# Kernel tuning notes

Measured on AMD Instinct MI355X. Metric: run time of the kernel, lower is better.

## Reference

```python
import jax, jax.numpy as jnp
import numpy as np

FACTORS = (16, 8, 8)          # prod == n_embd == 1024
H, DK = 16, 64
FACTOR_PARAMS = tuple(f * (f - 1) // 2 for f in FACTORS)  # (120, 28, 28)
DV = sum(FACTOR_PARAMS)       # 176
DVP = 256                     # next power of two padding
B, T, C = 2, 2048, 1024
OFFSET = 64


def _skew_exp(params, f):
    """params: (..., f*(f-1)//2) -> rotation matrices (..., f, f) via expm of skew-sym."""
    rows, cols = np.triu_indices(f, k=1)
    batch = params.shape[:-1]
    mat = jnp.zeros(batch + (f, f), jnp.float32).at[..., rows, cols].set(params.astype(jnp.float32))
    S = mat - jnp.swapaxes(mat, -1, -2)
    R = jax.vmap(jax.scipy.linalg.expm)(S.reshape((-1, f, f)))
    return R.reshape(batch + (f, f))


def setup_inputs() -> dict:
    key = jax.random.key(0)
    k1, k2, k3, k4, k5 = jax.random.split(key, 5)
    return {
        "x": jax.random.normal(k1, (B, T, C), jnp.float32),
        "cached_k": jax.random.normal(k2, (B, H, OFFSET, DK), jnp.float32),
        "cached_v": jax.random.normal(k3, (B, H, OFFSET, DVP), jnp.float32),
        "W_QK": jax.random.normal(k4, (2 * H * DK, C), jnp.float32) * 0.02,
        "W_V": jax.random.normal(k5, (H * DV, C), jnp.float32) * 0.02,
    }


def reference(x, cached_k, cached_v, W_QK, W_V):
    Bx, Tx, Cx = x.shape
    qk = x @ W_QK.T                                  # (B,T,2*H*DK)
    q, k = jnp.split(qk, 2, axis=-1)
    q = q.reshape(Bx, Tx, H, DK).transpose(0, 2, 1, 3)   # (B,H,T,DK)
    k = k.reshape(Bx, Tx, H, DK).transpose(0, 2, 1, 3)
    v = (x @ W_V.T).reshape(Bx, Tx, H, DV).transpose(0, 2, 1, 3)  # (B,H,T,DV)
    v = jnp.pad(v, ((0, 0), (0, 0), (0, 0), (0, DVP - DV)))       # pad to DVP

    offset = cached_k.shape[2]
    k = jnp.concatenate([cached_k, k], axis=2)       # (B,H,offset+T,DK)
    v = jnp.concatenate([cached_v, v], axis=2)       # (B,H,offset+T,DVP)

    neg_inf = jnp.finfo(jnp.float32).min
    causal = jnp.triu(jnp.full((Tx, Tx), neg_inf, jnp.float32), k=1)
    mask = jnp.concatenate([jnp.zeros((Tx, offset), jnp.float32), causal], axis=1)

    scores = jnp.einsum('bhqd,bhkd->bhqk', q, k) * (1.0 / np.sqrt(DK)) + mask
    attn = jax.nn.softmax(scores, axis=-1)
    rot = jnp.einsum('bhqk,bhkd->bhqd', attn, v)[..., :DV]   # (B,H,T,DV)
    rot = rot.transpose(0, 2, 1, 3).sum(axis=2)              # sum over heads -> (B,T,DV)

    splits = jnp.split(rot, np.cumsum(FACTOR_PARAMS)[:-1].tolist(), axis=-1)
    y = x.reshape(Bx, Tx, *FACTORS)
    for i, (p, f) in enumerate(zip(splits, FACTORS)):
        R = _skew_exp(p, f).astype(x.dtype)          # (B,T,f,f)
        y = jnp.moveaxis(y, 2 + i, 2)
        sh = y.shape
        y = (R @ y.reshape(Bx, Tx, f, -1)).reshape(sh)
        y = jnp.moveaxis(y, 2, 2 + i)
    y = y.reshape(Bx, Tx, Cx)
    return y, k, v
```

## Files before the change

### kernel.cpp

```cpp
#include <hip/hip_runtime.h>

typedef _Float16 h8 __attribute__((ext_vector_type(8)));
typedef _Float16 h4 __attribute__((ext_vector_type(4)));
typedef float f4 __attribute__((ext_vector_type(4)));

#define NB 2
#define NT 2048
#define NC 1024
#define NH 16
#define DKK 64
#define DV 176
#define DVP 256
#define OFF 64
#define KV 2112
#define SCALE_Q 0.18033688011112f
#define CLAMP_S 11.541560327111f

__device__ __forceinline__ void load_lds16(const _Float16* g, _Float16* l) {
    __builtin_amdgcn_global_load_lds(
        (const __attribute__((address_space(1))) void*)g,
        (__attribute__((address_space(3))) void*)l, 16, 0, 0);
}

#define PREPA_X   1048576
#define PREPA_QK  1572864
#define PREPA_WV  2293760
#define PREPA_END 2473984
__global__ __launch_bounds__(256)
void k_prep_a(const float* __restrict__ x, const float* __restrict__ wqk,
              const float* __restrict__ wv, _Float16* __restrict__ xh,
              _Float16* __restrict__ wqkh, _Float16* __restrict__ wvh,
              float* __restrict__ rotb) {
    int i = blockIdx.x * 256 + threadIdx.x;
    if (i >= PREPA_END) return;
    if (i < PREPA_X) {
        float4 v = *(const float4*)(x + (size_t)i * 4);
        h4 h = {(_Float16)v.x, (_Float16)v.y, (_Float16)v.z, (_Float16)v.w};
        *(h4*)(xh + (size_t)i * 4) = h;
    } else if (i < PREPA_QK) {
        int j = i - PREPA_X;
        float4 v = *(const float4*)(wqk + (size_t)j * 4);
        h4 h = {(_Float16)v.x, (_Float16)v.y, (_Float16)v.z, (_Float16)v.w};
        *(h4*)(wqkh + (size_t)j * 4) = h;
    } else if (i < PREPA_WV) {
        int j = i - PREPA_QK;
        float4 v = *(const float4*)(wv + (size_t)j * 4);
        h4 h = {(_Float16)v.x, (_Float16)v.y, (_Float16)v.z, (_Float16)v.w};
        *(h4*)(wvh + (size_t)j * 4) = h;
    } else {
        int j = i - PREPA_WV;
        *(float4*)(rotb + (size_t)j * 4) = (float4){0.f, 0.f, 0.f, 0.f};
    }
}

#define PREPB_CK   32768
#define PREPB_CV   163840
#define PREPB_END  1474560
__global__ __launch_bounds__(256)
void k_prep_b(const float* __restrict__ ck, const float* __restrict__ cv,
              float* __restrict__ out_k, _Float16* __restrict__ kh,
              float* __restrict__ out_v, _Float16* __restrict__ vTh) {
    int i = blockIdx.x * 256 + threadIdx.x;
    if (i >= PREPB_END) return;
    if (i < PREPB_CK) {
        int bh = i >> 10, rem = i & 1023;
        int pos = rem >> 4, d4 = (rem & 15) * 4;
        float4 v = *(const float4*)(ck + (size_t)i * 4);
        size_t o = ((size_t)bh * KV + pos) * DKK + d4;
        *(float4*)(out_k + o) = v;
        h4 h = {(_Float16)v.x, (_Float16)v.y, (_Float16)v.z, (_Float16)v.w};
        *(h4*)(kh + o) = h;
    } else if (i < PREPB_CV) {
        int j = i - PREPB_CK;
        int bh = j >> 12, rem = j & 4095;
        int pos = rem >> 6, c4 = (rem & 63) * 4;
        float4 v = *(const float4*)(cv + (size_t)j * 4);
        *(float4*)(out_v + ((size_t)bh * KV + pos) * DVP + c4) = v;
        if (c4 < DV) {
            _Float16* vt = vTh + ((size_t)bh * DV + c4) * KV + pos;
            vt[0]              = (_Float16)v.x;
            vt[KV]             = (_Float16)v.y;
            vt[2 * (size_t)KV] = (_Float16)v.z;
            vt[3 * (size_t)KV] = (_Float16)v.w;
        }
    } else {
        int j = i - PREPB_CV;
        int bh = j / 40960, rem = j - bh * 40960;
        int t = rem / 20, c4 = DV + (rem - t * 20) * 4;
        *(float4*)(out_v + ((size_t)bh * KV + OFF + t) * DVP + c4) = (float4){0.f, 0.f, 0.f, 0.f};
    }
}

__global__ __launch_bounds__(256)
void k_gemm_fused(const _Float16* __restrict__ xh, const _Float16* __restrict__ wh,
                  _Float16* __restrict__ qh, _Float16* __restrict__ kh,
                  float* __restrict__ out_k, _Float16* __restrict__ vTh,
                  float* __restrict__ out_v) {
    __shared__ char smem_raw[65536];
    auto Ts = (_Float16(*)[64][72])smem_raw;
    auto Tq = (_Float16(*)[128][68])smem_raw;

    const int tid = threadIdx.x;
    const int lane = tid & 63, w = tid >> 6;
    const int lr = lane & 15, lg = lane >> 4;
    const int wm = w >> 1, wn = w & 1;
    const int n = blockIdx.x, x = n & 7, idx = n >> 3;
    const int c_  = idx >> 6;
    const int loc = idx & 63;
    const int mi = (x & 3) * 8 + (loc & 7);
    const int ni = (x >> 2) * 19 + c_ * 8 + (loc >> 3);
    const int m0 = mi * 128, n0 = ni * 128;
    const int srow = lane >> 3;
    const int sc16 = (lane & 7) ^ srow;

    f4 acc[4][4];
#pragma unroll
    for (int i = 0; i < 4; i++)
#pragma unroll
        for (int j = 0; j < 4; j++) acc[i][j] = (f4){0.f, 0.f, 0.f, 0.f};

    auto stage = [&](int buf, int k0) {
        _Float16* Ab = (_Float16*)smem_raw + buf * 8192;
        _Float16* Bb = (_Float16*)(smem_raw + 32768) + buf * 8192;
#pragma unroll
        for (int j = 0; j < 4; j++) {
            int i = w * 4 + j;
            int row = i * 8 + srow;
            load_lds16(&xh[(size_t)(m0 + row) * NC + k0 + sc16 * 8], Ab + i * 512);
            load_lds16(&wh[(size_t)(n0 + row) * NC + k0 + sc16 * 8], Bb + i * 512);
        }
    };

    stage(0, 0);
    int cur = 0;
    for (int t = 0; t < 16; ++t) {
        if (t < 15) {
            stage(cur ^ 1, (t + 1) * 64);
            asm volatile("s_waitcnt vmcnt(8)" ::: "memory");
        } else {
            asm volatile("s_waitcnt vmcnt(0)" ::: "memory");
        }
        __builtin_amdgcn_s_barrier();
        __builtin_amdgcn_sched_barrier(0);

        const _Float16* Ab = (const _Float16*)smem_raw + cur * 8192;
        const _Float16* Bb = (const _Float16*)(smem_raw + 32768) + cur * 8192;
#pragma unroll
        for (int ks = 0; ks < 2; ks++) {
            h8 a[4], b[4];
#pragma unroll
            for (int mt = 0; mt < 4; mt++) {
                int row = wm * 64 + mt * 16 + lr;
                a[mt] = *(const h8*)&Ab[row * 64 + ((ks * 4 + lg) ^ (lr & 7)) * 8];
            }
#pragma unroll
            for (int nt = 0; nt < 4; nt++) {
                int row = wn * 64 + nt * 16 + lr;
                b[nt] = *(const h8*)&Bb[row * 64 + ((ks * 4 + lg) ^ (lr & 7)) * 8];
            }
            __builtin_amdgcn_s_setprio(1);
#pragma unroll
            for (int mt = 0; mt < 4; mt++)
#pragma unroll
                for (int nt = 0; nt < 4; nt++)
                    acc[mt][nt] = __builtin_amdgcn_mfma_f32_16x16x32_f16(a[mt], b[nt], acc[mt][nt], 0, 0, 0);
            __builtin_amdgcn_s_setprio(0);
        }
        __builtin_amdgcn_sched_barrier(0);
        __builtin_amdgcn_s_barrier();
        cur ^= 1;
    }

    const int b_ = m0 >> 11;
    const int mloc = m0 & (NT - 1);

    if (ni < 8) {
        __syncthreads();
#pragma unroll
        for (int mt = 0; mt < 4; mt++)
#pragma unroll
            for (int nt = 0; nt < 4; nt++)
#pragma unroll
                for (int r = 0; r < 4; r++)
                    Tq[wn][wm * 64 + mt * 16 + lg * 4 + r][nt * 16 + lr] =
                        (_Float16)(acc[mt][nt][r] * SCALE_Q);
        __syncthreads();
        const int h0 = n0 >> 6;
#pragma unroll
        for (int i = 0; i < 8; i++) {
            int id = i * 256 + tid;
            int hh = id >> 10, rem = id & 1023;
            int t = rem >> 3, dk8 = (rem & 7) * 8;
            h8 v = *(const h8*)&Tq[hh][t][dk8];
            *(h8*)&qh[((size_t)(b_ * NH + h0 + hh) * NT + mloc + t) * DKK + dk8] = v;
        }
    } else if (ni < 16) {
        __syncthreads();
#pragma unroll
        for (int mt = 0; mt < 4; mt++)
#pragma unroll
            for (int nt = 0; nt < 4; nt++)
#pragma unroll
                for (int r = 0; r < 4; r++) {
                    int t = wm * 64 + mt * 16 + lg * 4 + r;
                    int g2 = n0 - 1024 + wn * 64 + nt * 16 + lr;
                    float v = acc[mt][nt][r];
                    int h = g2 >> 6, dk = g2 & 63;
                    out_k[((size_t)(b_ * NH + h) * KV + OFF + mloc + t) * DKK + dk] = v;
                    Tq[wn][t][nt * 16 + lr] = (_Float16)v;
                }
        __syncthreads();
        const int h0 = (n0 - 1024) >> 6;
#pragma unroll
        for (int i = 0; i < 8; i++) {
            int id = i * 256 + tid;
            int hh = id >> 10, rem = id & 1023;
            int t = rem >> 3, dk8 = (rem & 7) * 8;
            h8 v = *(const h8*)&Tq[hh][t][dk8];
            *(h8*)&kh[((size_t)(b_ * NH + h0 + hh) * KV + OFF + mloc + t) * DKK + dk8] = v;
        }
    } else {
        __syncthreads();
#pragma unroll
        for (int mt = 0; mt < 4; mt++)
#pragma unroll
            for (int nt = 0; nt < 4; nt++) {
                h4 ph;
#pragma unroll
                for (int r = 0; r < 4; r++) {
                    int grow = m0 + wm * 64 + mt * 16 + lg * 4 + r;
                    int gcol = n0 - 2048 + wn * 64 + nt * 16 + lr;
                    float v = acc[mt][nt][r];
                    int bb = grow >> 11, t = grow & (NT - 1);
                    int h = gcol / DV;
                    int c = gcol - h * DV;
                    out_v[((size_t)(bb * NH + h) * KV + OFF + t) * DVP + c] = v;
                    ph[r] = (_Float16)v;
                }
                *(h4*)&Ts[w][nt * 16 + lr][mt * 16 + lg * 4] = ph;
            }
        __syncthreads();
        {
            _Float16* vout = vTh + ((size_t)b_ * (NH * DV) + (n0 - 2048)) * KV + OFF + mloc;
            const int seg = tid & 31;
            const int rr = tid >> 5;
#pragma unroll
            for (int i = 0; i < 16; i++) {
                int c = i * 8 + rr;
                int buf = ((seg >> 4) << 1) | (c >> 6);
                h4 vv = *(const h4*)&Ts[buf][c & 63][(seg & 15) * 4];
                *(h4*)&vout[(size_t)c * KV + seg * 4] = vv;
            }
        }
    }
}

__global__ __launch_bounds__(256, 2)
void k_attn(const _Float16* __restrict__ qh, const _Float16* __restrict__ kh,
            const _Float16* __restrict__ vTh, float* __restrict__ rot) {
    __shared__ _Float16 Ks[2][64][64];
    __shared__ _Float16 Vs[2][176][64];
    __shared__ _Float16 Ps[4][16][72];
    const int tid = threadIdx.x, lane = tid & 63, w = tid >> 6;
    const int lr = lane & 15, lg = lane >> 4;
    const int n = blockIdx.x;
    const int gq = 31 - (n >> 5);
    const int bh = (n & 7) + 8 * ((n >> 3) & 3);
    const int b_ = bh >> 4;
    const int qt = gq * 4 + w;
    const int q = qt * 16 + lr;

    const _Float16* qp = qh + ((size_t)bh * NT + q) * DKK;
    h8 bq0 = *(const h8*)(qp + lg * 8);
    h8 bq1 = *(const h8*)(qp + 32 + lg * 8);

    const _Float16* kbase = kh + (size_t)bh * KV * DKK;
    const _Float16* vbase = vTh + (size_t)bh * DV * KV;

    f4 o[11];
#pragma unroll
    for (int i = 0; i < 11; i++) o[i] = (f4){0.f, 0.f, 0.f, 0.f};
    float l_acc = 0.f;

    const int nkt = gq + 2;
    const int srow = lane >> 3, sslot = lane & 7;
    const int sc16 = sslot ^ srow;

    auto stage = [&](int buf, int kt) {
#pragma unroll
        for (int t = 0; t < 8; t++) {
            int i = w * 8 + t;
            if (i > 29) i = 29;
            if (i < 8) {
                int row = i * 8 + srow;
                load_lds16(&kbase[(size_t)(kt * 64 + row) * DKK + sc16 * 8],
                           (_Float16*)Ks[buf] + i * 512);
            } else {
                int j = i - 8;
                int row = j * 8 + srow;
                load_lds16(&vbase[(size_t)row * KV + kt * 64 + sc16 * 8],
                           (_Float16*)Vs[buf] + j * 512);
            }
        }
    };

    stage(0, 0);
    int cur = 0;

    for (int kt = 0; kt < nkt; kt++) {
        if (kt + 1 < nkt) {
            stage(cur ^ 1, kt + 1);
            asm volatile("s_waitcnt vmcnt(8)" ::: "memory");
        } else {
            asm volatile("s_waitcnt vmcnt(0)" ::: "memory");
        }
        __builtin_amdgcn_s_barrier();
        __builtin_amdgcn_sched_barrier(0);

        f4 s[4];
        __builtin_amdgcn_s_setprio(1);
#pragma unroll
        for (int nt = 0; nt < 4; nt++) {
            int krow = nt * 16 + lr;
            h8 ak0 = *(const h8*)&Ks[cur][krow][(lg ^ (lr & 7)) * 8];
            h8 ak1 = *(const h8*)&Ks[cur][krow][((4 + lg) ^ (lr & 7)) * 8];
            f4 st = (f4){0.f, 0.f, 0.f, 0.f};
            st = __builtin_amdgcn_mfma_f32_16x16x32_f16(ak0, bq0, st, 0, 0, 0);
            st = __builtin_amdgcn_mfma_f32_16x16x32_f16(ak1, bq1, st, 0, 0, 0);
            s[nt] = st;
        }
        __builtin_amdgcn_s_setprio(0);

        if (kt + 1 < nkt) {
#pragma unroll
            for (int nt = 0; nt < 4; nt++) {
                h4 ph;
#pragma unroll
                for (int r = 0; r < 4; r++) {
                    float p = __builtin_exp2f(fminf(s[nt][r], CLAMP_S));
                    l_acc += p;
                    ph[r] = (_Float16)p;
                }
                *(h4*)&Ps[w][lr][nt * 16 + lg * 4] = ph;
            }
        } else {
#pragma unroll
            for (int nt = 0; nt < 4; nt++) {
                h4 ph;
#pragma unroll
                for (int r = 0; r < 4; r++) {
                    int key = kt * 64 + nt * 16 + lg * 4 + r;
                    float sv = fminf(s[nt][r], CLAMP_S);
                    float p = (key <= q + OFF) ? __builtin_exp2f(sv) : 0.f;
                    l_acc += p;
                    ph[r] = (_Float16)p;
                }
                *(h4*)&Ps[w][lr][nt * 16 + lg * 4] = ph;
            }
        }

        __builtin_amdgcn_s_setprio(1);
#pragma unroll
        for (int ks = 0; ks < 2; ks++) {
            h8 ap = *(const h8*)&Ps[w][lr][ks * 32 + lg * 8];
#pragma unroll
            for (int nt = 0; nt < 11; nt++) {
                int vrow = nt * 16 + lr;
                h8 bv = *(const h8*)&Vs[cur][vrow][((ks * 4 + lg) ^ (lr & 7)) * 8];
                o[nt] = __builtin_amdgcn_mfma_f32_16x16x32_f16(ap, bv, o[nt], 0, 0, 0);
            }
        }
        __builtin_amdgcn_s_setprio(0);
        __builtin_amdgcn_sched_barrier(0);
        __builtin_amdgcn_s_barrier();
        cur ^= 1;
    }

    l_acc += __shfl_xor(l_acc, 16);
    l_acc += __shfl_xor(l_acc, 32);
    float lq[4];
#pragma unroll
    for (int r = 0; r < 4; r++) lq[r] = 1.f / __shfl(l_acc, lg * 4 + r);
#pragma unroll
    for (int r = 0; r < 4; r++) {
        int t = qt * 16 + lg * 4 + r;
#pragma unroll
        for (int nt = 0; nt < 11; nt++) {
            atomicAdd(&rot[((size_t)b_ * NT + t) * DV + nt * 16 + lr], o[nt][r] * lq[r]);
        }
    }
}

__device__ __forceinline__ int triu16(int r, int c) { return r * 15 - (r * (r - 1)) / 2 + (c - r - 1); }
__device__ __forceinline__ int triu8(int r, int c)  { return r * 7  - (r * (r - 1)) / 2 + (c - r - 1); }

__global__ __launch_bounds__(64)
void k_rotate(const float* __restrict__ x, const float* __restrict__ rot,
              float* __restrict__ y) {
    __shared__ float A16[16][16], Ta[16][16], Tb[16][16];
    __shared__ float A8[2][8][8], T8a[2][8][8], T8b[2][8][8];
    __shared__ float pbuf[176];
    __shared__ float xt[1024], t1[1024], t2[1024];
    const int tok = blockIdx.x;
    const int lane = threadIdx.x;

    for (int i = lane; i < 176; i += 64) pbuf[i] = rot[(size_t)tok * DV + i];
    for (int i = lane; i < 1024; i += 64) xt[i] = x[(size_t)tok * NC + i];
    __syncthreads();

#pragma unroll
    for (int j = 0; j < 4; j++) {
        int e = lane * 4 + j, r = e >> 4, c = e & 15;
        float v = 0.f;
        if (r < c) v = pbuf[triu16(r, c)];
        else if (r > c) v = -pbuf[triu16(c, r)];
        A16[r][c] = v;
    }
    const int r8 = lane >> 3, c8 = lane & 7;
    {
#pragma unroll
        for (int m = 0; m < 2; m++) {
            float v = 0.f;
            if (r8 < c8) v = pbuf[120 + m * 28 + triu8(r8, c8)];
            else if (r8 > c8) v = -pbuf[120 + m * 28 + triu8(c8, r8)];
            A8[m][r8][c8] = v;
        }
    }
    __syncthreads();

    float rn = 0.f;
    if (lane < 16) {
#pragma unroll
        for (int c = 0; c < 16; c++) rn += fabsf(A16[lane][c]);
    }
#pragma unroll
    for (int mm = 1; mm < 16; mm <<= 1) rn = fmaxf(rn, __shfl_xor(rn, mm));
    rn = __shfl(rn, 0);
    int s16 = 0;
    while (rn > 0.5f && s16 < 60) { rn *= 0.5f; s16++; }

    int s8v[2];
#pragma unroll
    for (int m = 0; m < 2; m++) {
        float rn8 = 0.f;
        if (lane < 8) {
#pragma unroll
            for (int cc = 0; cc < 8; cc++) rn8 += fabsf(A8[m][lane][cc]);
        }
#pragma unroll
        for (int mm = 1; mm < 8; mm <<= 1) rn8 = fmaxf(rn8, __shfl_xor(rn8, mm));
        rn8 = __shfl(rn8, 0);
        int s8 = 0;
        while (rn8 > 0.5f && s8 < 60) { rn8 *= 0.5f; s8++; }
        s8v[m] = s8;
    }
    const float sc16 = exp2f((float)(-s16));
    const float sc80 = exp2f((float)(-s8v[0]));
    const float sc81 = exp2f((float)(-s8v[1]));
    __syncthreads();

#pragma unroll
    for (int j = 0; j < 4; j++) {
        int e = lane * 4 + j, r = e >> 4, c = e & 15;
        A16[r][c] *= sc16;
    }
    A8[0][r8][c8] *= sc80;
    A8[1][r8][c8] *= sc81;
    __syncthreads();
#pragma unroll
    for (int j = 0; j < 4; j++) {
        int e = lane * 4 + j, r = e >> 4, c = e & 15;
        Ta[r][c] = (r == c ? 1.f : 0.f) + A16[r][c] * (1.f / 12.f);
    }
    T8a[0][r8][c8] = (r8 == c8 ? 1.f : 0.f) + A8[0][r8][c8] * (1.f / 12.f);
    T8a[1][r8][c8] = (r8 == c8 ? 1.f : 0.f) + A8[1][r8][c8] * (1.f / 12.f);
    __syncthreads();

    float (*Tc)[16] = Ta, (*Tn)[16] = Tb;
    float (*tc0)[8] = T8a[0], (*tn0)[8] = T8b[0];
    float (*tc1)[8] = T8a[1], (*tn1)[8] = T8b[1];

    for (int k = 11; k >= 1; k--) {
        float inv_k = 1.f / (float)k;
#pragma unroll
        for (int j = 0; j < 4; j++) {
            int e = lane * 4 + j, r = e >> 4, c = e & 15;
            float acc = 0.f;
#pragma unroll
            for (int qv = 0; qv < 16; qv++) acc += A16[r][qv] * Tc[qv][c];
            Tn[r][c] = acc * inv_k + (r == c ? 1.f : 0.f);
        }
        {
            float a0 = 0.f, a1 = 0.f;
#pragma unroll
            for (int qv = 0; qv < 8; qv++) {
                a0 += A8[0][r8][qv] * tc0[qv][c8];
                a1 += A8[1][r8][qv] * tc1[qv][c8];
            }
            tn0[r8][c8] = a0 * inv_k + (r8 == c8 ? 1.f : 0.f);
            tn1[r8][c8] = a1 * inv_k + (r8 == c8 ? 1.f : 0.f);
        }
        __syncthreads();
        { float (*t)[16] = Tc; Tc = Tn; Tn = t; }
        { float (*t)[8] = tc0; tc0 = tn0; tn0 = t; }
        { float (*t)[8] = tc1; tc1 = tn1; tn1 = t; }
    }

    int smax = s16 > s8v[0] ? s16 : s8v[0];
    if (s8v[1] > smax) smax = s8v[1];
    for (int it = 0; it < smax; it++) {
        if (it < s16) {
#pragma unroll
            for (int j = 0; j < 4; j++) {
                int e = lane * 4 + j, r = e >> 4, c = e & 15;
                float acc = 0.f;
#pragma unroll
                for (int qv = 0; qv < 16; qv++) acc += Tc[r][qv] * Tc[qv][c];
                Tn[r][c] = acc;
            }
        }
        if (it < s8v[0]) {
            float a0 = 0.f;
#pragma unroll
            for (int qv = 0; qv < 8; qv++) a0 += tc0[r8][qv] * tc0[qv][c8];
            tn0[r8][c8] = a0;
        }
        if (it < s8v[1]) {
            float a1 = 0.f;
#pragma unroll
            for (int qv = 0; qv < 8; qv++) a1 += tc1[r8][qv] * tc1[qv][c8];
            tn1[r8][c8] = a1;
        }
        __syncthreads();
        if (it < s16) { float (*t)[16] = Tc; Tc = Tn; Tn = t; }
        if (it < s8v[0]) { float (*t)[8] = tc0; tc0 = tn0; tn0 = t; }
        if (it < s8v[1]) { float (*t)[8] = tc1; tc1 = tn1; tn1 = t; }
    }
    float (*R2p)[8] = tc0;
    float (*R3p)[8] = tc1;
    __syncthreads();

    for (int o = lane; o < 1024; o += 64) {
        int c = o & 7, base = o & ~7;
        float acc = 0.f;
#pragma unroll
        for (int j = 0; j < 8; j++) acc += R3p[c][j] * xt[base + j];
        t1[o] = acc;
    }
    __syncthreads();
    for (int o = lane; o < 1024; o += 64) {
        int c = o & 7, bb = (o >> 3) & 7, a = o >> 6;
        float acc = 0.f;
#pragma unroll
        for (int j = 0; j < 8; j++) acc += R2p[bb][j] * t1[a * 64 + j * 8 + c];
        t2[o] = acc;
    }
    __syncthreads();
    for (int o = lane; o < 1024; o += 64) {
        int rr = o & 63, a = o >> 6;
        float acc = 0.f;
#pragma unroll
        for (int j = 0; j < 16; j++) acc += Tc[a][j] * t2[j * 64 + rr];
        y[(size_t)tok * NC + o] = acc;
    }
}

extern "C" void kernel_launch(void* const* d_in, const int* in_sizes, int n_in,
                              void* d_out, int out_size, void* d_ws, size_t ws_size,
                              hipStream_t stream) {
    const float* x   = (const float*)d_in[0];
    const float* ck  = (const float*)d_in[1];
    const float* cv  = (const float*)d_in[2];
    const float* wqk = (const float*)d_in[3];
    const float* wv  = (const float*)d_in[4];

    float* out_y = (float*)d_out;
    float* out_k = out_y + (size_t)NB * NT * NC;
    float* out_v = out_k + (size_t)NB * NH * KV * DKK;

    char* ws = (char*)d_ws;
    _Float16* xh   = (_Float16*)ws;  ws += (size_t)NB * NT * NC * 2;
    _Float16* wqkh = (_Float16*)ws;  ws += (size_t)2 * NH * DKK * NC * 2;
    _Float16* wvh  = (_Float16*)ws;  ws += (size_t)NH * DV * NC * 2;
    _Float16* qh   = (_Float16*)ws;  ws += (size_t)NB * NH * NT * DKK * 2;
    _Float16* kh   = (_Float16*)ws;  ws += (size_t)NB * NH * KV * DKK * 2;
    _Float16* vTh  = (_Float16*)ws;  ws += (size_t)NB * NH * DV * KV * 2;
    float*    rotb = (float*)ws;     ws += (size_t)NB * NT * DV * 4;

    k_prep_a<<<dim3((PREPA_END + 255) / 256), dim3(256), 0, stream>>>(
        x, wqk, wv, xh, wqkh, wvh, rotb);
    k_prep_b<<<dim3((PREPB_END + 255) / 256), dim3(256), 0, stream>>>(
        ck, cv, out_k, kh, out_v, vTh);

    k_gemm_fused<<<dim3(1216), dim3(256), 0, stream>>>(xh, wqkh, qh, kh, out_k, vTh, out_v);

    k_attn<<<dim3(1024), dim3(256), 0, stream>>>(qh, kh, vTh, rotb);

    k_rotate<<<dim3(NB * NT), dim3(64), 0, stream>>>(x, rotb, out_y);
}
```

Measured before the change: 196.2 us.

## Replace double-buffered LDS async loads with register-staged single buffer in attention

The attention kernel drops its double-buffered LDS tiles for K and V and the direct global-to-LDS loads. Next-tile data is now prefetched into registers while the current tile is computed, then written to a single LDS buffer at the top of each iteration. Halving LDS use lets the launch bound request four blocks per CU instead of two, trading extra VGPRs and an LDS write and wait step per iteration for higher occupancy.

```diff
diff --git a/kernel.cpp b/kernel.cpp
--- a/kernel.cpp
+++ b/kernel.cpp
@@ -255,11 +255,11 @@
     }
 }
 
-__global__ __launch_bounds__(256, 2)
+__global__ __launch_bounds__(256, 4)
 void k_attn(const _Float16* __restrict__ qh, const _Float16* __restrict__ kh,
             const _Float16* __restrict__ vTh, float* __restrict__ rot) {
-    __shared__ _Float16 Ks[2][64][64];
-    __shared__ _Float16 Vs[2][176][64];
+    __shared__ _Float16 Ks[64][64];
+    __shared__ _Float16 Vs[176][64];
     __shared__ _Float16 Ps[4][16][72];
     const int tid = threadIdx.x, lane = tid & 63, w = tid >> 6;
     const int lr = lane & 15, lg = lane >> 4;
@@ -286,44 +286,53 @@
     const int srow = lane >> 3, sslot = lane & 7;
     const int sc16 = sslot ^ srow;
 
-    auto stage = [&](int buf, int kt) {
-#pragma unroll
-        for (int t = 0; t < 8; t++) {
-            int i = w * 8 + t;
-            if (i > 29) i = 29;
-            if (i < 8) {
+    h8 rk[2], rv[6];
+    auto issue = [&](int kt) {
+#pragma unroll
+        for (int j = 0; j < 2; j++) {
+            int i = w * 2 + j;
+            int row = i * 8 + srow;
+            rk[j] = *(const h8*)&kbase[(size_t)(kt * 64 + row) * DKK + sc16 * 8];
+        }
+#pragma unroll
+        for (int j = 0; j < 6; j++) {
+            int i = w * 6 + j;
+            if (i < 22) {
                 int row = i * 8 + srow;
-                load_lds16(&kbase[(size_t)(kt * 64 + row) * DKK + sc16 * 8],
-                           (_Float16*)Ks[buf] + i * 512);
-            } else {
-                int j = i - 8;
-                int row = j * 8 + srow;
-                load_lds16(&vbase[(size_t)row * KV + kt * 64 + sc16 * 8],
-                           (_Float16*)Vs[buf] + j * 512);
+                rv[j] = *(const h8*)&vbase[(size_t)row * KV + kt * 64 + sc16 * 8];
             }
         }
     };
-
-    stage(0, 0);
-    int cur = 0;
+    auto publish = [&]() {
+#pragma unroll
+        for (int j = 0; j < 2; j++) {
+            int i = w * 2 + j;
+            *(h8*)((_Float16*)Ks + i * 512 + lane * 8) = rk[j];
+        }
+#pragma unroll
+        for (int j = 0; j < 6; j++) {
+            int i = w * 6 + j;
+            if (i < 22) *(h8*)((_Float16*)Vs + i * 512 + lane * 8) = rv[j];
+        }
+    };
+
+    issue(0);
 
     for (int kt = 0; kt < nkt; kt++) {
-        if (kt + 1 < nkt) {
-            stage(cur ^ 1, kt + 1);
-            asm volatile("s_waitcnt vmcnt(8)" ::: "memory");
-        } else {
-            asm volatile("s_waitcnt vmcnt(0)" ::: "memory");
-        }
+        publish();
+        asm volatile("s_waitcnt lgkmcnt(0)" ::: "memory");
         __builtin_amdgcn_s_barrier();
         __builtin_amdgcn_sched_barrier(0);
+        if (kt + 1 < nkt) issue(kt + 1);
+        __builtin_amdgcn_sched_barrier(0);
 
         f4 s[4];
         __builtin_amdgcn_s_setprio(1);
 #pragma unroll
         for (int nt = 0; nt < 4; nt++) {
             int krow = nt * 16 + lr;
-            h8 ak0 = *(const h8*)&Ks[cur][krow][(lg ^ (lr & 7)) * 8];
-            h8 ak1 = *(const h8*)&Ks[cur][krow][((4 + lg) ^ (lr & 7)) * 8];
+            h8 ak0 = *(const h8*)&Ks[krow][(lg ^ (lr & 7)) * 8];
+            h8 ak1 = *(const h8*)&Ks[krow][((4 + lg) ^ (lr & 7)) * 8];
             f4 st = (f4){0.f, 0.f, 0.f, 0.f};
             st = __builtin_amdgcn_mfma_f32_16x16x32_f16(ak0, bq0, st, 0, 0, 0);
             st = __builtin_amdgcn_mfma_f32_16x16x32_f16(ak1, bq1, st, 0, 0, 0);
@@ -366,14 +375,13 @@
 #pragma unroll
             for (int nt = 0; nt < 11; nt++) {
                 int vrow = nt * 16 + lr;
-                h8 bv = *(const h8*)&Vs[cur][vrow][((ks * 4 + lg) ^ (lr & 7)) * 8];
+                h8 bv = *(const h8*)&Vs[vrow][((ks * 4 + lg) ^ (lr & 7)) * 8];
                 o[nt] = __builtin_amdgcn_mfma_f32_16x16x32_f16(ap, bv, o[nt], 0, 0, 0);
             }
         }
         __builtin_amdgcn_s_setprio(0);
         __builtin_amdgcn_sched_barrier(0);
         __builtin_amdgcn_s_barrier();
-        cur ^= 1;
     }
 
     l_acc += __shfl_xor(l_acc, 16);
```

Result: slower. 234.6 us (+19.6%).
